# Performance work log

Measured on AMD Instinct MI355X. Metric: run time of the kernel, lower is better.

The kernel has to match this reference:

```python
import jax, jax.numpy as jnp
import numpy as np

N_HEAD = 16
NEG = -1e9


def setup_inputs() -> dict:
    key = jax.random.key(0)
    ks = jax.random.split(key, 10)
    b, s, f = 4, 1024, 1024
    h = N_HEAD
    scale = 1.0 / np.sqrt(f).astype(np.float32)
    x = jax.random.normal(ks[0], (b, s, f), jnp.float32)
    str_mat = jax.random.normal(ks[1], (b, h, s, s), jnp.float32)
    # causal binary mask, float as in the torch module (attn_mask == 0.0 test)
    attn_mask = jnp.broadcast_to(jnp.tril(jnp.ones((s, s), jnp.float32))[None, None], (b, 1, s, s))
    Wq = jax.random.normal(ks[2], (f, f), jnp.float32) * scale
    Wk = jax.random.normal(ks[3], (f, f), jnp.float32) * scale
    Wv = jax.random.normal(ks[4], (f, f), jnp.float32) * scale
    Wo = jax.random.normal(ks[5], (f, f), jnp.float32) * scale
    bq = jax.random.normal(ks[6], (f,), jnp.float32) * 0.01
    bk = jax.random.normal(ks[7], (f,), jnp.float32) * 0.01
    bv = jax.random.normal(ks[8], (f,), jnp.float32) * 0.01
    bo = jax.random.normal(ks[9], (f,), jnp.float32) * 0.01
    return {"x": x, "str_mat": str_mat, "attn_mask": attn_mask,
            "Wq": Wq, "bq": bq, "Wk": Wk, "bk": bk,
            "Wv": Wv, "bv": bv, "Wo": Wo, "bo": bo}


def reference(x, str_mat, attn_mask, Wq, bq, Wk, bk, Wv, bv, Wo, bo):
    b, s, f = x.shape
    h = N_HEAD
    d_h = f // h
    # NOTE: original uses .view(b, h, -1, d_h) with NO transpose -> raw reshape
    q = (x @ Wq + bq).reshape(b, h, s, d_h)
    k = (x @ Wk + bk).reshape(b, h, s, d_h)
    v = (x @ Wv + bv).reshape(b, h, s, d_h)
    # structural bias: mask then softmax
    sm = jnp.where(attn_mask == 0.0, NEG, str_mat)
    sm = jax.nn.softmax(sm, axis=-1)
    # scale by d_h (NOT sqrt(d_h)) as in source; second masked_fill in source
    # is non-in-place with result discarded -> no-op, intentionally omitted
    scores = jnp.einsum('bhqd,bhkd->bhqk', q, k) / d_h + sm
    prob = jax.nn.softmax(scores, axis=-1)  # dropout p=0.0
    out = jnp.einsum('bhqk,bhkd->bhqd', prob, v)  # [b,h,s,d_h]
    out = out.transpose(0, 2, 1, 3).reshape(b, s, f)
    return out @ Wo + bo
```

## Files before the change

kernel.cpp:

```cpp
#include <hip/hip_runtime.h>
#include <hip/hip_bf16.h>

#define BB 4
#define SS 1024
#define FF 1024
#define HH 16
#define DH 64

typedef short bf16x8 __attribute__((ext_vector_type(8)));
typedef float f32x4 __attribute__((ext_vector_type(4)));

__device__ __forceinline__ float b2f(unsigned short u) {
    union { unsigned int i; float f; } x; x.i = ((unsigned int)u) << 16; return x.f;
}
__device__ __forceinline__ unsigned short f2b(float f) {
    unsigned int x = __float_as_uint(f);
    unsigned int r = (x + 0x7fffu + ((x >> 16) & 1u)) >> 16;
    return (unsigned short)r;
}
__device__ __forceinline__ int sw(int row, int col) { return col ^ ((row & 7) << 3); }

__global__ void cvt_k(const float* __restrict__ in, unsigned short* __restrict__ out, int n) {
    int i = (blockIdx.x * blockDim.x + threadIdx.x) * 4;
    if (i < n) {
        float4 v = *(const float4*)(in + i);
        ushort4 o;
        o.x = f2b(v.x); o.y = f2b(v.y); o.z = f2b(v.z); o.w = f2b(v.w);
        *(ushort4*)(out + i) = o;
    }
}

__global__ void cvtT_k(const float* __restrict__ W0, const float* __restrict__ W1,
                       const float* __restrict__ W2, const float* __restrict__ W3,
                       unsigned short* __restrict__ out) {
    int y = blockIdx.y;
    const float* src = (y == 0) ? W0 : (y == 1) ? W1 : (y == 2) ? W2 : W3;
    unsigned short* dst = out + (size_t)y * FF * FF;
    __shared__ float t[32][33];
    int tile = blockIdx.x;
    int tk = (tile & 31) * 32, tn = (tile >> 5) * 32;
    int r = threadIdx.x >> 3, c4 = (threadIdx.x & 7) * 4;
    float4 v = *(const float4*)&src[(size_t)(tk + r) * FF + tn + c4];
    t[r][c4 + 0] = v.x; t[r][c4 + 1] = v.y; t[r][c4 + 2] = v.z; t[r][c4 + 3] = v.w;
    __syncthreads();
    ushort4 o;
    o.x = f2b(t[c4 + 0][r]); o.y = f2b(t[c4 + 1][r]);
    o.z = f2b(t[c4 + 2][r]); o.w = f2b(t[c4 + 3][r]);
    *(ushort4*)&dst[(size_t)(tn + r) * FF + tk + c4] = o;
}

__global__ void vtrans_k(const unsigned short* __restrict__ V, unsigned short* __restrict__ Vt) {
    int bh = blockIdx.y;
    int sb = blockIdx.x * 64;
    size_t slab = (size_t)bh * SS * DH;
    __shared__ unsigned int tI[64][65];
    int tid = threadIdx.x;
    #pragma unroll
    for (int v = 0; v < 2; v++) {
        int c = tid + v * 256;
        int row = c >> 3, col = (c & 7) * 8;
        uint4 u = *(const uint4*)&V[slab + (size_t)(sb + row) * DH + col];
        const unsigned short* us = (const unsigned short*)&u;
        #pragma unroll
        for (int j = 0; j < 8; j++) tI[row][col + j] = us[j];
    }
    __syncthreads();
    #pragma unroll
    for (int v = 0; v < 2; v++) {
        int c = tid + v * 256;
        int drow = c >> 3, scol = (c & 7) * 8;
        unsigned short o[8];
        #pragma unroll
        for (int j = 0; j < 8; j++) o[j] = (unsigned short)tI[scol + j][drow];
        *(uint4*)&Vt[slab + (size_t)drow * SS + sb + scol] = *(uint4*)o;
    }
}

__global__ __launch_bounds__(256, 1) void gemm_k(
    const unsigned short* __restrict__ A, const unsigned short* __restrict__ Wt,
    const float* __restrict__ b0, const float* __restrict__ b1, const float* __restrict__ b2,
    unsigned short* __restrict__ o16, float* __restrict__ o32, int mode)
{
    __shared__ __attribute__((aligned(16))) unsigned short lA[2][128 * 64];
    __shared__ __attribute__((aligned(16))) unsigned short lB[2][128 * 64];

    int tid = threadIdx.x;
    int wave = tid >> 6, lane = tid & 63, quad = lane >> 4, l16 = lane & 15;
    int wm = (wave & 1) * 64, wn = (wave >> 1) * 64;
    int mbase = blockIdx.x * 128;
    int srow = tid >> 3, scol = (tid & 7) * 8;

    int nbase;
    const float* bias;
    float scale = 1.0f;
    const unsigned short* W = Wt;
    unsigned short* oq = o16;
    if (mode == 1) {
        int widx = blockIdx.y >> 3;
        nbase = (blockIdx.y & 7) * 128;
        W = Wt + (size_t)widx * FF * FF;
        bias = (widx == 0) ? b0 : (widx == 1) ? b1 : b2;
        scale = (widx == 0) ? 0.015625f : 1.0f;
        oq = o16 + (size_t)widx * BB * SS * FF;
    } else {
        nbase = blockIdx.y * 128;
        bias = b0;
    }

    f32x4 acc[4][4];
    #pragma unroll
    for (int i = 0; i < 4; i++)
        #pragma unroll
        for (int j = 0; j < 4; j++) acc[i][j] = (f32x4){0.f, 0.f, 0.f, 0.f};

    const unsigned short* pA = A + (size_t)(mbase + srow) * FF + scol;
    const unsigned short* pB = W + (size_t)(nbase + srow) * FF + scol;

    uint4 ra[4], rb[4];
    #pragma unroll
    for (int i = 0; i < 4; i++) {
        ra[i] = *(const uint4*)(pA + (size_t)i * 32 * FF);
        rb[i] = *(const uint4*)(pB + (size_t)i * 32 * FF);
    }
    #pragma unroll
    for (int i = 0; i < 4; i++) {
        *(uint4*)&lA[0][(srow + i * 32) * 64 + sw(srow, scol)] = ra[i];
        *(uint4*)&lB[0][(srow + i * 32) * 64 + sw(srow, scol)] = rb[i];
    }
    __syncthreads();

    for (int kt = 0; kt < 16; kt++) {
        int cur = kt & 1;
        if (kt < 15) {
            #pragma unroll
            for (int i = 0; i < 4; i++) {
                ra[i] = *(const uint4*)(pA + (kt + 1) * 64 + (size_t)i * 32 * FF);
                rb[i] = *(const uint4*)(pB + (kt + 1) * 64 + (size_t)i * 32 * FF);
            }
        }
        #pragma unroll
        for (int ks = 0; ks < 2; ks++) {
            bf16x8 af[4], bfr[4];
            #pragma unroll
            for (int mi = 0; mi < 4; mi++) {
                int row = wm + mi * 16 + l16;
                af[mi] = *(const bf16x8*)(&lA[cur][row * 64 + sw(row, ks * 32 + quad * 8)]);
            }
            #pragma unroll
            for (int ni = 0; ni < 4; ni++) {
                int row = wn + ni * 16 + l16;
                bfr[ni] = *(const bf16x8*)(&lB[cur][row * 64 + sw(row, ks * 32 + quad * 8)]);
            }
            #pragma unroll
            for (int mi = 0; mi < 4; mi++)
                #pragma unroll
                for (int ni = 0; ni < 4; ni++)
                    acc[mi][ni] = __builtin_amdgcn_mfma_f32_16x16x32_bf16(af[mi], bfr[ni], acc[mi][ni], 0, 0, 0);
        }
        if (kt < 15) {
            #pragma unroll
            for (int i = 0; i < 4; i++) {
                *(uint4*)&lA[cur ^ 1][(srow + i * 32) * 64 + sw(srow, scol)] = ra[i];
                *(uint4*)&lB[cur ^ 1][(srow + i * 32) * 64 + sw(srow, scol)] = rb[i];
            }
        }
        __syncthreads();
    }

    #pragma unroll
    for (int mi = 0; mi < 4; mi++) {
        #pragma unroll
        for (int ni = 0; ni < 4; ni++) {
            int col = nbase + wn + ni * 16 + l16;
            float bv = bias[col];
            #pragma unroll
            for (int r = 0; r < 4; r++) {
                int row = mbase + wm + mi * 16 + quad * 4 + r;
                float v = (acc[mi][ni][r] + bv) * scale;
                if (mode == 1) {
                    int b_ = row >> 10, i = row & 1023;
                    int h = i >> 6, s_ = ((i & 63) << 4) + (col >> 6), d = col & 63;
                    oq[(((size_t)(b_ * HH + h)) * SS + s_) * DH + d] = f2b(v);
                } else {
                    o32[(size_t)row * FF + col] = v;
                }
            }
        }
    }
}

__global__ void rowstats_k(const float* __restrict__ str,
                           float* __restrict__ rmax, float* __restrict__ rinv) {
    int row = blockIdx.x * 4 + (threadIdx.x >> 6);
    int lane = threadIdx.x & 63;
    int r = row & (SS - 1);
    const float* p = str + (size_t)row * SS;
    float vals[16];
    float mx = -1e30f;
    #pragma unroll
    for (int i = 0; i < 4; i++) {
        int k0 = i * 256 + lane * 4;
        float4 u = *(const float4*)(&p[k0]);
        float uv[4] = {u.x, u.y, u.z, u.w};
        #pragma unroll
        for (int j = 0; j < 4; j++) {
            float v = (k0 + j <= r) ? uv[j] : -1e30f;
            vals[i * 4 + j] = v;
            mx = fmaxf(mx, v);
        }
    }
    #pragma unroll
    for (int d = 1; d < 64; d <<= 1) mx = fmaxf(mx, __shfl_xor(mx, d));
    float sum = 0.f;
    #pragma unroll
    for (int i = 0; i < 16; i++) sum += __expf(fminf(vals[i] - mx, 0.f));
    #pragma unroll
    for (int d = 1; d < 64; d <<= 1) sum += __shfl_xor(sum, d);
    if (lane == 0) { rmax[row] = mx; rinv[row] = 1.0f / sum; }
}

__global__ __launch_bounds__(256, 2) void attn_k(
    const unsigned short* __restrict__ Q, const unsigned short* __restrict__ K,
    const unsigned short* __restrict__ Vt, const float* __restrict__ str,
    const float* __restrict__ rmax, const float* __restrict__ rinv,
    unsigned short* __restrict__ ctx)
{
    int bh = blockIdx.y;
    int b_ = bh >> 4, h = bh & 15;
    int qbase = blockIdx.x * 64;
    int tid = threadIdx.x;
    int wave = tid >> 6, lane = tid & 63, quad = lane >> 4, l16 = lane & 15;
    int srow = tid >> 3, scol = (tid & 7) * 8;

    __shared__ __attribute__((aligned(16))) unsigned short lQP[64 * 64];
    __shared__ __attribute__((aligned(16))) unsigned short lK[2][64 * 64];
    __shared__ __attribute__((aligned(16))) unsigned short lV[2][64 * 64];

    const size_t slab = (size_t)bh * SS * DH;

    #pragma unroll
    for (int v = 0; v < 2; v++) {
        int row = srow + v * 32;
        *(uint4*)&lQP[row * 64 + sw(row, scol)]   = *(const uint4*)&Q [slab + (size_t)(qbase + row) * DH + scol];
        *(uint4*)&lK[0][row * 64 + sw(row, scol)] = *(const uint4*)&K [slab + (size_t)row * DH + scol];
        *(uint4*)&lV[0][row * 64 + sw(row, scol)] = *(const uint4*)&Vt[slab + (size_t)row * SS + scol];
    }
    int q_loc0 = wave * 16 + quad * 4;
    float rm4[4], ri4[4];
    #pragma unroll
    for (int r = 0; r < 4; r++) {
        rm4[r] = rmax[bh * SS + qbase + q_loc0 + r];
        ri4[r] = rinv[bh * SS + qbase + q_loc0 + r];
    }
    __syncthreads();

    bf16x8 aq[2];
    #pragma unroll
    for (int ks = 0; ks < 2; ks++) {
        int row = wave * 16 + l16;
        aq[ks] = *(const bf16x8*)&lQP[row * 64 + sw(row, ks * 32 + quad * 8)];
    }

    float m_st[4], l_st[4];
    f32x4 Oacc[4];
    #pragma unroll
    for (int r = 0; r < 4; r++) { m_st[r] = -1e30f; l_st[r] = 0.f; }
    #pragma unroll
    for (int ni = 0; ni < 4; ni++) Oacc[ni] = (f32x4){0.f, 0.f, 0.f, 0.f};

    const size_t strbase = (size_t)bh * SS * SS;
    unsigned short* lPw = &lQP[(wave * 16) * 64];

    for (int tt = 0; tt < 16; tt++) {
        int cur = tt & 1;
        int tbase = tt * 64;
        bool need_sm = (tbase <= qbase + 63);

        float sf[4][4];
        if (need_sm) {
            #pragma unroll
            for (int r = 0; r < 4; r++) {
                int q_abs = qbase + q_loc0 + r;
                int lim = q_abs - tbase;
                const float* pr = str + strbase + (size_t)q_abs * SS + tbase + l16;
                #pragma unroll
                for (int ni = 0; ni < 4; ni++)
                    sf[ni][r] = (ni * 16 + l16 <= lim) ? pr[ni * 16] : -1e30f;
            }
        }
        uint4 kst[2], vst[2];
        if (tt < 15) {
            #pragma unroll
            for (int v = 0; v < 2; v++) {
                int row = srow + v * 32;
                kst[v] = *(const uint4*)&K [slab + (size_t)(tbase + 64 + row) * DH + scol];
                vst[v] = *(const uint4*)&Vt[slab + (size_t)row * SS + tbase + 64 + scol];
            }
        }

        f32x4 sa[4];
        #pragma unroll
        for (int ni = 0; ni < 4; ni++) sa[ni] = (f32x4){0.f, 0.f, 0.f, 0.f};
        #pragma unroll
        for (int ks = 0; ks < 2; ks++) {
            #pragma unroll
            for (int ni = 0; ni < 4; ni++) {
                int row = ni * 16 + l16;
                bf16x8 bk_ = *(const bf16x8*)&lK[cur][row * 64 + sw(row, ks * 32 + quad * 8)];
                sa[ni] = __builtin_amdgcn_mfma_f32_16x16x32_bf16(aq[ks], bk_, sa[ni], 0, 0, 0);
            }
        }

        float tm[4];
        #pragma unroll
        for (int r = 0; r < 4; r++) tm[r] = -1e30f;
        #pragma unroll
        for (int ni = 0; ni < 4; ni++) {
            #pragma unroll
            for (int r = 0; r < 4; r++) {
                float v = sa[ni][r];
                if (need_sm)
                    v += __expf(fminf(sf[ni][r] - rm4[r], 0.f)) * ri4[r];
                sa[ni][r] = v;
                tm[r] = fmaxf(tm[r], v);
            }
        }
        #pragma unroll
        for (int r = 0; r < 4; r++) {
            float v = tm[r];
            v = fmaxf(v, __shfl_xor(v, 1));
            v = fmaxf(v, __shfl_xor(v, 2));
            v = fmaxf(v, __shfl_xor(v, 4));
            v = fmaxf(v, __shfl_xor(v, 8));
            tm[r] = v;
        }
        float alpha[4], rs[4];
        #pragma unroll
        for (int r = 0; r < 4; r++) {
            float mn = fmaxf(m_st[r], tm[r]);
            alpha[r] = __expf(fminf(m_st[r] - mn, 0.f));
            m_st[r] = mn;
            rs[r] = 0.f;
        }
        #pragma unroll
        for (int ni = 0; ni < 4; ni++)
            #pragma unroll
            for (int r = 0; r < 4; r++) {
                sa[ni][r] = __expf(fminf(sa[ni][r] - m_st[r], 0.f));
                rs[r] += sa[ni][r];
            }
        #pragma unroll
        for (int r = 0; r < 4; r++) {
            float v = rs[r];
            v += __shfl_xor(v, 1); v += __shfl_xor(v, 2);
            v += __shfl_xor(v, 4); v += __shfl_xor(v, 8);
            l_st[r] = l_st[r] * alpha[r] + v;
        }
        #pragma unroll
        for (int ni = 0; ni < 4; ni++)
            #pragma unroll
            for (int r = 0; r < 4; r++) Oacc[ni][r] *= alpha[r];

        #pragma unroll
        for (int ni = 0; ni < 4; ni++)
            #pragma unroll
            for (int r = 0; r < 4; r++) {
                int pr = quad * 4 + r;
                lPw[pr * 64 + sw(pr, ni * 16 + l16)] = f2b(sa[ni][r]);
            }

        #pragma unroll
        for (int ks = 0; ks < 2; ks++) {
            bf16x8 pa = *(const bf16x8*)&lPw[l16 * 64 + sw(l16, ks * 32 + quad * 8)];
            #pragma unroll
            for (int ni = 0; ni < 4; ni++) {
                int row = ni * 16 + l16;
                bf16x8 bv = *(const bf16x8*)&lV[cur][row * 64 + sw(row, ks * 32 + quad * 8)];
                Oacc[ni] = __builtin_amdgcn_mfma_f32_16x16x32_bf16(pa, bv, Oacc[ni], 0, 0, 0);
            }
        }

        if (tt < 15) {
            #pragma unroll
            for (int v = 0; v < 2; v++) {
                int row = srow + v * 32;
                *(uint4*)&lK[cur ^ 1][row * 64 + sw(row, scol)] = kst[v];
                *(uint4*)&lV[cur ^ 1][row * 64 + sw(row, scol)] = vst[v];
            }
        }
        __syncthreads();
    }

    #pragma unroll
    for (int r = 0; r < 4; r++) {
        int s_abs = qbase + wave * 16 + quad * 4 + r;
        float li = 1.0f / l_st[r];
        #pragma unroll
        for (int ni = 0; ni < 4; ni++) {
            int d = ni * 16 + l16;
            ctx[((size_t)b_ * SS + s_abs) * FF + h * 64 + d] = f2b(Oacc[ni][r] * li);
        }
    }
}

extern "C" void kernel_launch(void* const* d_in, const int* in_sizes, int n_in,
                              void* d_out, int out_size, void* d_ws, size_t ws_size,
                              hipStream_t stream) {
    const float* x   = (const float*)d_in[0];
    const float* str = (const float*)d_in[1];
    const float* Wq  = (const float*)d_in[3];
    const float* bq  = (const float*)d_in[4];
    const float* Wk  = (const float*)d_in[5];
    const float* bk  = (const float*)d_in[6];
    const float* Wv  = (const float*)d_in[7];
    const float* bv  = (const float*)d_in[8];
    const float* Wo  = (const float*)d_in[9];
    const float* bo  = (const float*)d_in[10];

    char* ws = (char*)d_ws;
    const size_t MB = 1024ull * 1024;
    unsigned short* xb  = (unsigned short*)ws;
    unsigned short* Wb  = (unsigned short*)(ws + 8 * MB);
    unsigned short* QKV = (unsigned short*)(ws + 16 * MB);
    unsigned short* Vtp = (unsigned short*)(ws + 40 * MB);
    unsigned short* ctx = (unsigned short*)(ws + 48 * MB);
    float* rmax = (float*)(ws + 56 * MB);
    float* rinv = (float*)(ws + 56 * MB + 256 * 1024);

    const size_t QN = (size_t)BB * SS * FF;
    const size_t WN = (size_t)FF * FF;

    cvt_k<<<4096, 256, 0, stream>>>(x, xb, (int)QN);
    cvtT_k<<<dim3(1024, 4), 256, 0, stream>>>(Wq, Wk, Wv, Wo, Wb);

    gemm_k<<<dim3(32, 24), 256, 0, stream>>>(xb, Wb, bq, bk, bv, QKV, nullptr, 1);
    vtrans_k<<<dim3(16, 64), 256, 0, stream>>>(QKV + 2 * QN, Vtp);
    rowstats_k<<<16384, 256, 0, stream>>>(str, rmax, rinv);
    attn_k<<<dim3(16, 64), 256, 0, stream>>>(QKV, QKV + QN, Vtp, str, rmax, rinv, ctx);
    gemm_k<<<dim3(32, 8), 256, 0, stream>>>(ctx, Wb + 3 * WN, bo, nullptr, nullptr, nullptr, (float*)d_out, 0);
}
```

Baseline: 557.1 us.

## Use async global-to-LDS loads, precompute bf16 structural softmax, remap workgroups

The GEMM and attention kernels now stage K/V and A/B tiles with global_load_lds direct-to-LDS copies instead of going through registers. The gemm launch bound rises to 2 and attn_k to 4 waves per SIMD. Both kernels remap block IDs to group work per XCD. The rowstats kernel is replaced by one that writes the normalized structural softmax as bf16 and skips fully masked column chunks. attn_k then reads half-size bf16 values and drops the per-element exp. This trades an extra 128MB write plus a later read, and some bf16 rounding of the bias, for less traffic and compute inside attention.

```diff
diff --git a/kernel.cpp b/kernel.cpp
--- a/kernel.cpp
+++ b/kernel.cpp
@@ -19,6 +19,12 @@
     return (unsigned short)r;
 }
 __device__ __forceinline__ int sw(int row, int col) { return col ^ ((row & 7) << 3); }
+
+__device__ __forceinline__ void async_copy16(void* lds, const void* g) {
+    __builtin_amdgcn_global_load_lds(
+        (const __attribute__((address_space(1))) unsigned int*)g,
+        (__attribute__((address_space(3))) unsigned int*)lds, 16, 0, 0);
+}
 
 __global__ void cvt_k(const float* __restrict__ in, unsigned short* __restrict__ out, int n) {
     int i = (blockIdx.x * blockDim.x + threadIdx.x) * 4;
@@ -76,7 +82,7 @@
     }
 }
 
-__global__ __launch_bounds__(256, 1) void gemm_k(
+__global__ __launch_bounds__(256, 2) void gemm_k(
     const unsigned short* __restrict__ A, const unsigned short* __restrict__ Wt,
     const float* __restrict__ b0, const float* __restrict__ b1, const float* __restrict__ b2,
     unsigned short* __restrict__ o16, float* __restrict__ o32, int mode)
@@ -87,8 +93,16 @@
     int tid = threadIdx.x;
     int wave = tid >> 6, lane = tid & 63, quad = lane >> 4, l16 = lane & 15;
     int wm = (wave & 1) * 64, wn = (wave >> 1) * 64;
-    int mbase = blockIdx.x * 128;
     int srow = tid >> 3, scol = (tid & 7) * 8;
+    int scolsw = scol ^ ((srow & 7) << 3);
+    int wv = wave;
+
+    int gy = gridDim.y;
+    int bid = blockIdx.y * gridDim.x + blockIdx.x;
+    int chunk = (gridDim.x * gy) >> 3;
+    int wgid = (bid & 7) * chunk + (bid >> 3);
+    int mi_ = wgid / gy, nc = wgid - mi_ * gy;
+    int mbase = mi_ * 128;
 
     int nbase;
     const float* bias;
@@ -96,14 +110,14 @@
     const unsigned short* W = Wt;
     unsigned short* oq = o16;
     if (mode == 1) {
-        int widx = blockIdx.y >> 3;
-        nbase = (blockIdx.y & 7) * 128;
+        int widx = nc >> 3;
+        nbase = (nc & 7) * 128;
         W = Wt + (size_t)widx * FF * FF;
         bias = (widx == 0) ? b0 : (widx == 1) ? b1 : b2;
         scale = (widx == 0) ? 0.015625f : 1.0f;
         oq = o16 + (size_t)widx * BB * SS * FF;
     } else {
-        nbase = blockIdx.y * 128;
+        nbase = nc * 128;
         bias = b0;
     }
 
@@ -113,29 +127,24 @@
         #pragma unroll
         for (int j = 0; j < 4; j++) acc[i][j] = (f32x4){0.f, 0.f, 0.f, 0.f};
 
-    const unsigned short* pA = A + (size_t)(mbase + srow) * FF + scol;
-    const unsigned short* pB = W + (size_t)(nbase + srow) * FF + scol;
-
-    uint4 ra[4], rb[4];
+    const unsigned short* gA = A + (size_t)(mbase + srow) * FF + scolsw;
+    const unsigned short* gB = W + (size_t)(nbase + srow) * FF + scolsw;
+
     #pragma unroll
     for (int i = 0; i < 4; i++) {
-        ra[i] = *(const uint4*)(pA + (size_t)i * 32 * FF);
-        rb[i] = *(const uint4*)(pB + (size_t)i * 32 * FF);
-    }
-    #pragma unroll
-    for (int i = 0; i < 4; i++) {
-        *(uint4*)&lA[0][(srow + i * 32) * 64 + sw(srow, scol)] = ra[i];
-        *(uint4*)&lB[0][(srow + i * 32) * 64 + sw(srow, scol)] = rb[i];
+        async_copy16((void*)&lA[0][(i * 32 + wv * 8) * 64], gA + (size_t)i * 32 * FF);
+        async_copy16((void*)&lB[0][(i * 32 + wv * 8) * 64], gB + (size_t)i * 32 * FF);
     }
     __syncthreads();
 
     for (int kt = 0; kt < 16; kt++) {
         int cur = kt & 1;
         if (kt < 15) {
+            int kb = (kt + 1) * 64;
             #pragma unroll
             for (int i = 0; i < 4; i++) {
-                ra[i] = *(const uint4*)(pA + (kt + 1) * 64 + (size_t)i * 32 * FF);
-                rb[i] = *(const uint4*)(pB + (kt + 1) * 64 + (size_t)i * 32 * FF);
+                async_copy16((void*)&lA[cur ^ 1][(i * 32 + wv * 8) * 64], gA + (size_t)i * 32 * FF + kb);
+                async_copy16((void*)&lB[cur ^ 1][(i * 32 + wv * 8) * 64], gB + (size_t)i * 32 * FF + kb);
             }
         }
         #pragma unroll
@@ -156,13 +165,6 @@
                 #pragma unroll
                 for (int ni = 0; ni < 4; ni++)
                     acc[mi][ni] = __builtin_amdgcn_mfma_f32_16x16x32_bf16(af[mi], bfr[ni], acc[mi][ni], 0, 0, 0);
-        }
-        if (kt < 15) {
-            #pragma unroll
-            for (int i = 0; i < 4; i++) {
-                *(uint4*)&lA[cur ^ 1][(srow + i * 32) * 64 + sw(srow, scol)] = ra[i];
-                *(uint4*)&lB[cur ^ 1][(srow + i * 32) * 64 + sw(srow, scol)] = rb[i];
-            }
         }
         __syncthreads();
     }
@@ -189,48 +191,73 @@
     }
 }
 
-__global__ void rowstats_k(const float* __restrict__ str,
-                           float* __restrict__ rmax, float* __restrict__ rinv) {
+__global__ void sm_k(const float* __restrict__ str, unsigned short* __restrict__ smq) {
     int row = blockIdx.x * 4 + (threadIdx.x >> 6);
     int lane = threadIdx.x & 63;
     int r = row & (SS - 1);
+    int imax = r >> 8;
     const float* p = str + (size_t)row * SS;
     float vals[16];
     float mx = -1e30f;
     #pragma unroll
     for (int i = 0; i < 4; i++) {
         int k0 = i * 256 + lane * 4;
-        float4 u = *(const float4*)(&p[k0]);
-        float uv[4] = {u.x, u.y, u.z, u.w};
-        #pragma unroll
-        for (int j = 0; j < 4; j++) {
-            float v = (k0 + j <= r) ? uv[j] : -1e30f;
-            vals[i * 4 + j] = v;
-            mx = fmaxf(mx, v);
+        if (i <= imax) {
+            float4 u = *(const float4*)(&p[k0]);
+            float uv[4] = {u.x, u.y, u.z, u.w};
+            #pragma unroll
+            for (int j = 0; j < 4; j++) {
+                float v = (k0 + j <= r) ? uv[j] : -1e30f;
+                vals[i * 4 + j] = v;
+                mx = fmaxf(mx, v);
+            }
+        } else {
+            #pragma unroll
+            for (int j = 0; j < 4; j++) vals[i * 4 + j] = -1e30f;
         }
     }
     #pragma unroll
     for (int d = 1; d < 64; d <<= 1) mx = fmaxf(mx, __shfl_xor(mx, d));
     float sum = 0.f;
     #pragma unroll
-    for (int i = 0; i < 16; i++) sum += __expf(fminf(vals[i] - mx, 0.f));
+    for (int t = 0; t < 16; t++) {
+        float e = __expf(fminf(vals[t] - mx, 0.f));
+        vals[t] = e;
+        sum += e;
+    }
     #pragma unroll
     for (int d = 1; d < 64; d <<= 1) sum += __shfl_xor(sum, d);
-    if (lane == 0) { rmax[row] = mx; rinv[row] = 1.0f / sum; }
-}
-
-__global__ __launch_bounds__(256, 2) void attn_k(
+    float rinv = 1.0f / sum;
+    unsigned short* q = smq + (size_t)row * SS;
+    #pragma unroll
+    for (int i = 0; i < 4; i++) {
+        if (i <= imax) {
+            ushort4 o;
+            o.x = f2b(vals[i * 4 + 0] * rinv);
+            o.y = f2b(vals[i * 4 + 1] * rinv);
+            o.z = f2b(vals[i * 4 + 2] * rinv);
+            o.w = f2b(vals[i * 4 + 3] * rinv);
+            *(ushort4*)(&q[i * 256 + lane * 4]) = o;
+        }
+    }
+}
+
+__global__ __launch_bounds__(256, 4) void attn_k(
     const unsigned short* __restrict__ Q, const unsigned short* __restrict__ K,
-    const unsigned short* __restrict__ Vt, const float* __restrict__ str,
-    const float* __restrict__ rmax, const float* __restrict__ rinv,
+    const unsigned short* __restrict__ Vt, const unsigned short* __restrict__ sm,
     unsigned short* __restrict__ ctx)
 {
-    int bh = blockIdx.y;
-    int b_ = bh >> 4, h = bh & 15;
-    int qbase = blockIdx.x * 64;
     int tid = threadIdx.x;
     int wave = tid >> 6, lane = tid & 63, quad = lane >> 4, l16 = lane & 15;
     int srow = tid >> 3, scol = (tid & 7) * 8;
+    int scolsw = scol ^ ((srow & 7) << 3);
+    int wv = wave;
+
+    int bid = blockIdx.y * gridDim.x + blockIdx.x;
+    int wgid = (bid & 7) * 128 + (bid >> 3);
+    int qb = wgid & 15, bh = wgid >> 4;
+    int b_ = bh >> 4, h = bh & 15;
+    int qbase = qb * 64;
 
     __shared__ __attribute__((aligned(16))) unsigned short lQP[64 * 64];
     __shared__ __attribute__((aligned(16))) unsigned short lK[2][64 * 64];
@@ -241,17 +268,11 @@
     #pragma unroll
     for (int v = 0; v < 2; v++) {
         int row = srow + v * 32;
-        *(uint4*)&lQP[row * 64 + sw(row, scol)]   = *(const uint4*)&Q [slab + (size_t)(qbase + row) * DH + scol];
-        *(uint4*)&lK[0][row * 64 + sw(row, scol)] = *(const uint4*)&K [slab + (size_t)row * DH + scol];
-        *(uint4*)&lV[0][row * 64 + sw(row, scol)] = *(const uint4*)&Vt[slab + (size_t)row * SS + scol];
+        *(uint4*)&lQP[row * 64 + sw(row, scol)] = *(const uint4*)&Q[slab + (size_t)(qbase + row) * DH + scol];
+        async_copy16((void*)&lK[0][(v * 32 + wv * 8) * 64], &K [slab + (size_t)row * DH + scolsw]);
+        async_copy16((void*)&lV[0][(v * 32 + wv * 8) * 64], &Vt[slab + (size_t)row * SS + scolsw]);
     }
     int q_loc0 = wave * 16 + quad * 4;
-    float rm4[4], ri4[4];
-    #pragma unroll
-    for (int r = 0; r < 4; r++) {
-        rm4[r] = rmax[bh * SS + qbase + q_loc0 + r];
-        ri4[r] = rinv[bh * SS + qbase + q_loc0 + r];
-    }
     __syncthreads();
 
     bf16x8 aq[2];
@@ -268,33 +289,32 @@
     #pragma unroll
     for (int ni = 0; ni < 4; ni++) Oacc[ni] = (f32x4){0.f, 0.f, 0.f, 0.f};
 
-    const size_t strbase = (size_t)bh * SS * SS;
+    const size_t smbase = (size_t)bh * SS * SS;
     unsigned short* lPw = &lQP[(wave * 16) * 64];
 
     for (int tt = 0; tt < 16; tt++) {
         int cur = tt & 1;
         int tbase = tt * 64;
-        bool need_sm = (tbase <= qbase + 63);
-
+        bool need_sm = (tbase <= qbase);
+
+        if (tt < 15) {
+            int nb = tbase + 64;
+            #pragma unroll
+            for (int v = 0; v < 2; v++) {
+                int row = srow + v * 32;
+                async_copy16((void*)&lK[cur ^ 1][(v * 32 + wv * 8) * 64], &K [slab + (size_t)(nb + row) * DH + scolsw]);
+                async_copy16((void*)&lV[cur ^ 1][(v * 32 + wv * 8) * 64], &Vt[slab + (size_t)row * SS + nb + scolsw]);
+            }
+        }
         float sf[4][4];
         if (need_sm) {
             #pragma unroll
             for (int r = 0; r < 4; r++) {
                 int q_abs = qbase + q_loc0 + r;
-                int lim = q_abs - tbase;
-                const float* pr = str + strbase + (size_t)q_abs * SS + tbase + l16;
+                const unsigned short* pr = sm + smbase + (size_t)q_abs * SS + tbase + l16;
                 #pragma unroll
                 for (int ni = 0; ni < 4; ni++)
-                    sf[ni][r] = (ni * 16 + l16 <= lim) ? pr[ni * 16] : -1e30f;
-            }
-        }
-        uint4 kst[2], vst[2];
-        if (tt < 15) {
-            #pragma unroll
-            for (int v = 0; v < 2; v++) {
-                int row = srow + v * 32;
-                kst[v] = *(const uint4*)&K [slab + (size_t)(tbase + 64 + row) * DH + scol];
-                vst[v] = *(const uint4*)&Vt[slab + (size_t)row * SS + tbase + 64 + scol];
+                    sf[ni][r] = b2f(pr[ni * 16]);
             }
         }
 
@@ -319,8 +339,7 @@
             #pragma unroll
             for (int r = 0; r < 4; r++) {
                 float v = sa[ni][r];
-                if (need_sm)
-                    v += __expf(fminf(sf[ni][r] - rm4[r], 0.f)) * ri4[r];
+                if (need_sm) v += sf[ni][r];
                 sa[ni][r] = v;
                 tm[r] = fmaxf(tm[r], v);
             }
@@ -380,14 +399,6 @@
             }
         }
 
-        if (tt < 15) {
-            #pragma unroll
-            for (int v = 0; v < 2; v++) {
-                int row = srow + v * 32;
-                *(uint4*)&lK[cur ^ 1][row * 64 + sw(row, scol)] = kst[v];
-                *(uint4*)&lV[cur ^ 1][row * 64 + sw(row, scol)] = vst[v];
-            }
-        }
         __syncthreads();
     }
 
@@ -424,8 +435,7 @@
     unsigned short* QKV = (unsigned short*)(ws + 16 * MB);
     unsigned short* Vtp = (unsigned short*)(ws + 40 * MB);
     unsigned short* ctx = (unsigned short*)(ws + 48 * MB);
-    float* rmax = (float*)(ws + 56 * MB);
-    float* rinv = (float*)(ws + 56 * MB + 256 * 1024);
+    unsigned short* smb = (unsigned short*)(ws + 64 * MB);
 
     const size_t QN = (size_t)BB * SS * FF;
     const size_t WN = (size_t)FF * FF;
@@ -435,7 +445,7 @@
 
     gemm_k<<<dim3(32, 24), 256, 0, stream>>>(xb, Wb, bq, bk, bv, QKV, nullptr, 1);
     vtrans_k<<<dim3(16, 64), 256, 0, stream>>>(QKV + 2 * QN, Vtp);
-    rowstats_k<<<16384, 256, 0, stream>>>(str, rmax, rinv);
-    attn_k<<<dim3(16, 64), 256, 0, stream>>>(QKV, QKV + QN, Vtp, str, rmax, rinv, ctx);
+    sm_k<<<16384, 256, 0, stream>>>(str, smb);
+    attn_k<<<dim3(16, 64), 256, 0, stream>>>(QKV, QKV + QN, Vtp, smb, ctx);
     gemm_k<<<dim3(32, 8), 256, 0, stream>>>(ctx, Wb + 3 * WN, bo, nullptr, nullptr, nullptr, (float*)d_out, 0);
 }
```

New measurement: 531.9 us. -4.5%, faster.
